# Optimization experiments

Hardware: AMD Instinct MI355X
Metric: run time of the kernel (lower is better)

The kernel has to match this reference:

```python
import jax, jax.numpy as jnp
import numpy as np

# Module config (mirrors PlateYoloBlock __init__)
IMAGE_W, IMAGE_H = 2048, 2048
GRID_SIZE = 8
GRID_W = IMAGE_W // GRID_SIZE  # 256
GRID_H = IMAGE_H // GRID_SIZE  # 256
BBOX_ATTRS = 13


def _xy_offset():
    # np.meshgrid(arange(grid_w), arange(grid_h)) stacked on axis=2 -> (grid_h, grid_w, 2)
    # [..., 0] = x (column) index, [..., 1] = y (row) index
    gx = jnp.arange(GRID_W, dtype=jnp.float32)
    gy = jnp.arange(GRID_H, dtype=jnp.float32)
    xx, yy = jnp.meshgrid(gx, gy)  # each (grid_h, grid_w)
    return jnp.stack([xx, yy], axis=-1)  # (grid_h, grid_w, 2)


def setup_inputs() -> dict:
    key = jax.random.key(0)
    coordinates = jax.random.normal(key, (32, BBOX_ATTRS, GRID_H, GRID_W), dtype=jnp.float32)
    return {"coordinates": coordinates}


def reference(coordinates) -> jnp.ndarray:
    # Inference path of PlateYoloBlock.forward (target=None):
    #   permute (B,13,H,W) -> (B,H,W,13)
    #   xy   = sigmoid(raw[..., :2]) + grid offset
    #   wh   = exp(raw[..., 2:4])
    #   conf = sigmoid(raw[..., -1])
    #   all-but-conf scaled by grid_size; reshape to (B, grid_w*grid_h, 13)
    b = coordinates.shape[0]
    c = jnp.transpose(coordinates, (0, 2, 3, 1))  # (B, grid_h, grid_w, 13)
    xy = jax.nn.sigmoid(c[..., :2]) + _xy_offset()[None]  # (B,H,W,2)
    wh = jnp.exp(c[..., 2:4])
    corners = c[..., 4:12]  # raw 4-corner coords, untouched by activations
    conf = jax.nn.sigmoid(c[..., 12:13])
    boxes = jnp.concatenate([xy, wh, corners], axis=-1) * jnp.float32(GRID_SIZE)
    out = jnp.concatenate([boxes, conf], axis=-1)  # (B,H,W,13)
    return out.reshape(b, GRID_W * GRID_H, BBOX_ATTRS)
```

## Files before the change

kernel.cpp:

```cpp
#include <hip/hip_runtime.h>


#define NB      32
#define NC      13
#define HW      65536
#define WIDTH   256
#define TILE    512
#define THREADS 256

__device__ __forceinline__ float sigmoidf_(float x) {
    return 1.0f / (1.0f + __expf(-x));
}

__global__ __launch_bounds__(THREADS) void plate_yolo_kernel(
        const float* __restrict__ in, float* __restrict__ out) {
    __shared__ float lds[TILE * NC];

    const int tid = threadIdx.x;
    const long long s0 = (long long)blockIdx.x * TILE;
    const int b = (int)(s0 >> 16);
    const int posBase = (int)(s0 & (HW - 1));
    const float* __restrict__ inB = in + (long long)b * NC * HW + posBase;

    #pragma unroll
    for (int k = 0; k < TILE / THREADS; ++k) {
        const int p = tid + k * THREADS;
        const int pos = posBase + p;
        const float fx = (float)(pos & (WIDTH - 1));
        const float fy = (float)(pos >> 8);
        #pragma unroll
        for (int c = 0; c < NC; ++c) {
            float v = inB[c * HW + p];
            float r;
            if (c == 0)                 r = (sigmoidf_(v) + fx) * 8.0f;
            else if (c == 1)            r = (sigmoidf_(v) + fy) * 8.0f;
            else if (c == 2 || c == 3)  r = __expf(v) * 8.0f;
            else if (c == 12)           r = sigmoidf_(v);
            else                        r = v * 8.0f;
            lds[p * NC + c] = r;
        }
    }
    __syncthreads();

    const float4* __restrict__ src = (const float4*)lds;
    float4* __restrict__ dst = (float4*)(out + s0 * NC);
    const int n4 = TILE * NC / 4;
    #pragma unroll
    for (int j = tid; j < n4; j += THREADS) {
        dst[j] = src[j];
    }
}

extern "C" void kernel_launch(void* const* d_in, const int* in_sizes, int n_in,
                              void* d_out, int out_size, void* d_ws, size_t ws_size,
                              hipStream_t stream) {
    const float* in = (const float*)d_in[0];
    float* out = (float*)d_out;
    const int blocks = (NB * HW) / TILE;
    plate_yolo_kernel<<<blocks, THREADS, 0, stream>>>(in, out);
}
```

Measured before the change: 190.4 us.

## Vectorize per-thread loads and LDS writes with four positions per thread

Each thread now handles four consecutive positions, loading each channel as a float4 and writing its 52 transposed outputs to LDS as 13 float4 stores. The tile grows to 1024 positions per block, halving the block count and doubling LDS use to 52 KB. This targets instruction count and the scalar strided LDS stores of the old layout. In exchange it raises register pressure and LDS footprint, which may cut occupancy on a purely bandwidth-bound kernel.

```diff
diff --git a/kernel.cpp b/kernel.cpp
--- a/kernel.cpp
+++ b/kernel.cpp
@@ -5,7 +5,7 @@
 #define NC      13
 #define HW      65536
 #define WIDTH   256
-#define TILE    512
+#define TILE    1024
 #define THREADS 256
 
 __device__ __forceinline__ float sigmoidf_(float x) {
@@ -14,7 +14,7 @@
 
 __global__ __launch_bounds__(THREADS) void plate_yolo_kernel(
         const float* __restrict__ in, float* __restrict__ out) {
-    __shared__ float lds[TILE * NC];
+    __shared__ __align__(16) float lds[TILE * NC];
 
     const int tid = threadIdx.x;
     const long long s0 = (long long)blockIdx.x * TILE;
@@ -22,33 +22,46 @@
     const int posBase = (int)(s0 & (HW - 1));
     const float* __restrict__ inB = in + (long long)b * NC * HW + posBase;
 
+    const int p4 = tid * 4;
+    float4 v[NC];
     #pragma unroll
-    for (int k = 0; k < TILE / THREADS; ++k) {
-        const int p = tid + k * THREADS;
-        const int pos = posBase + p;
-        const float fx = (float)(pos & (WIDTH - 1));
-        const float fy = (float)(pos >> 8);
+    for (int c = 0; c < NC; ++c)
+        v[c] = *(const float4*)(inB + c * HW + p4);
+
+    const int pos = posBase + p4;
+    const float fx0 = (float)(pos & (WIDTH - 1));
+    const float fy  = (float)(pos >> 8);
+
+    float4 o[NC];
+    float* flat = (float*)o;
+    #pragma unroll
+    for (int j = 0; j < 4; ++j) {
+        const float x = fx0 + (float)j;
         #pragma unroll
         for (int c = 0; c < NC; ++c) {
-            float v = inB[c * HW + p];
+            const float val = ((const float*)&v[c])[j];
             float r;
-            if (c == 0)                 r = (sigmoidf_(v) + fx) * 8.0f;
-            else if (c == 1)            r = (sigmoidf_(v) + fy) * 8.0f;
-            else if (c == 2 || c == 3)  r = __expf(v) * 8.0f;
-            else if (c == 12)           r = sigmoidf_(v);
-            else                        r = v * 8.0f;
-            lds[p * NC + c] = r;
+            if (c == 0)                 r = (sigmoidf_(val) + x) * 8.0f;
+            else if (c == 1)            r = (sigmoidf_(val) + fy) * 8.0f;
+            else if (c == 2 || c == 3)  r = __expf(val) * 8.0f;
+            else if (c == 12)           r = sigmoidf_(val);
+            else                        r = val * 8.0f;
+            flat[j * NC + c] = r;
         }
     }
+
+    float4* ldsBase = (float4*)(lds + tid * (4 * NC));
+    #pragma unroll
+    for (int q = 0; q < NC; ++q)
+        ldsBase[q] = o[q];
+
     __syncthreads();
 
     const float4* __restrict__ src = (const float4*)lds;
     float4* __restrict__ dst = (float4*)(out + s0 * NC);
-    const int n4 = TILE * NC / 4;
     #pragma unroll
-    for (int j = tid; j < n4; j += THREADS) {
-        dst[j] = src[j];
-    }
+    for (int j = 0; j < NC; ++j)
+        dst[j * THREADS + tid] = src[j * THREADS + tid];
 }
 
 extern "C" void kernel_launch(void* const* d_in, const int* in_sizes, int n_in,
```

Result: no change. 190.6 us (+0.1%).
